# Kernel tuning notes

Measured on AMD Instinct MI355X. Metric: run time of the kernel, lower is better.

The kernel has to match this reference:

```python
import jax, jax.numpy as jnp
import numpy as np

EPS = 1e-5
NUM_HEADS = 12


def setup_inputs() -> dict:
    key = jax.random.key(0)
    ks = jax.random.split(key, 4)
    B, S, E = 8, 1024, 768
    x = jax.random.normal(ks[0], (B, S, E), dtype=jnp.float32)
    ln_w = jnp.ones((E,), dtype=jnp.float32)
    ln_b = jnp.zeros((E,), dtype=jnp.float32)
    # PyTorch packed in-projection [3E, E]; scale ~ Xavier-ish
    in_proj_w = jax.random.normal(ks[1], (3 * E, E), dtype=jnp.float32) * (1.0 / np.sqrt(E))
    in_proj_b = jnp.zeros((3 * E,), dtype=jnp.float32)
    out_proj_w = jax.random.normal(ks[2], (E, E), dtype=jnp.float32) * (1.0 / np.sqrt(E))
    out_proj_b = jnp.zeros((E,), dtype=jnp.float32)
    return {"x": x, "ln_w": ln_w, "ln_b": ln_b,
            "in_proj_w": in_proj_w, "in_proj_b": in_proj_b,
            "out_proj_w": out_proj_w, "out_proj_b": out_proj_b}


def reference(x, ln_w, ln_b, in_proj_w, in_proj_b, out_proj_w, out_proj_b):
    B, S, E = x.shape
    H = NUM_HEADS
    D = E // H
    # LayerNorm over last dim (eps matches torch default 1e-5)
    mu = jnp.mean(x, axis=-1, keepdims=True)
    var = jnp.mean((x - mu) ** 2, axis=-1, keepdims=True)
    xn = (x - mu) * jax.lax.rsqrt(var + EPS) * ln_w + ln_b
    # Packed QKV projection: [B,S,3E]
    qkv = jnp.einsum('bse,fe->bsf', xn, in_proj_w) + in_proj_b
    q, k, v = jnp.split(qkv, 3, axis=-1)
    # [B,H,S,D]
    q = q.reshape(B, S, H, D).transpose(0, 2, 1, 3)
    k = k.reshape(B, S, H, D).transpose(0, 2, 1, 3)
    v = v.reshape(B, S, H, D).transpose(0, 2, 1, 3)
    scale = 1.0 / jnp.sqrt(jnp.asarray(D, dtype=x.dtype))
    # Explicit scores [B,H,S,S] — matches the non-flash need_weights path
    scores = jnp.einsum('bhqd,bhkd->bhqk', q * scale, k)
    attn = jax.nn.softmax(scores, axis=-1)
    ctx = jnp.einsum('bhqk,bhkd->bhqd', attn, v)  # [B,H,S,D]
    ctx = ctx.transpose(0, 2, 1, 3).reshape(B, S, E)
    out = jnp.einsum('bse,fe->bsf', ctx, out_proj_w) + out_proj_b
    return out
```

## Files before the change

### kernel.cpp

```cpp
#include <hip/hip_runtime.h>
#include <cstdint>

typedef _Float16 half8 __attribute__((ext_vector_type(8)));
typedef _Float16 half4v __attribute__((ext_vector_type(4)));
typedef float f32x4 __attribute__((ext_vector_type(4)));

#define AS1(p) (const __attribute__((address_space(1))) void*)(p)
#define AS3(p) (__attribute__((address_space(3))) void*)(p)

__device__ __forceinline__ void gl_lds16(const _Float16* g, _Float16* l) {
  __builtin_amdgcn_global_load_lds(AS1(g), AS3(l), 16, 0, 0);
}

__device__ __forceinline__ f32x4 mfma16(half8 a, half8 b, f32x4 c) {
  return __builtin_amdgcn_mfma_f32_16x16x32_f16(a, b, c, 0, 0, 0);
}

__global__ void conv_f32_f16(const float* __restrict__ s, _Float16* __restrict__ d, int n4) {
  int i = blockIdx.x * 256 + threadIdx.x;
  int stride = gridDim.x * 256;
  for (; i < n4; i += stride) {
    float4 v = ((const float4*)s)[i];
    half4v o = { (_Float16)v.x, (_Float16)v.y, (_Float16)v.z, (_Float16)v.w };
    *(half4v*)(d + (size_t)i * 4) = o;
  }
}

__global__ __launch_bounds__(256) void ln_kernel(const float* __restrict__ x,
    const float* __restrict__ g, const float* __restrict__ be, _Float16* __restrict__ xn) {
  const int row = blockIdx.x, tid = threadIdx.x;
  const float* xr = x + (size_t)row * 768;
  float v0 = xr[tid], v1 = xr[tid + 256], v2 = xr[tid + 512];
  float s = v0 + v1 + v2;
  float ss = v0 * v0 + v1 * v1 + v2 * v2;
  __shared__ float red[8];
  const int w = tid >> 6, l = tid & 63;
  #pragma unroll
  for (int o = 32; o > 0; o >>= 1) { s += __shfl_down(s, o); ss += __shfl_down(ss, o); }
  if (l == 0) { red[w] = s; red[4 + w] = ss; }
  __syncthreads();
  s  = red[0] + red[1] + red[2] + red[3];
  ss = red[4] + red[5] + red[6] + red[7];
  float mu = s * (1.0f / 768.0f);
  float var = ss * (1.0f / 768.0f) - mu * mu;
  float rs = rsqrtf(var + 1e-5f);
  _Float16* xo = xn + (size_t)row * 768;
  xo[tid]       = (_Float16)((v0 - mu) * rs * g[tid]       + be[tid]);
  xo[tid + 256] = (_Float16)((v1 - mu) * rs * g[tid + 256] + be[tid + 256]);
  xo[tid + 512] = (_Float16)((v2 - mu) * rs * g[tid + 512] + be[tid + 512]);
}

template<int EPI>
__global__ __launch_bounds__(256) void gemm_bt(
    const _Float16* __restrict__ A, const _Float16* __restrict__ Bw,
    const float* __restrict__ bias,
    _Float16* __restrict__ qh, _Float16* __restrict__ kh, _Float16* __restrict__ vh,
    float* __restrict__ outp, int M, int N, int K) {
  __shared__ _Float16 As[128 * 32];
  __shared__ _Float16 Bs[128 * 32];
  const int tid = threadIdx.x;
  const int w = tid >> 6, l = tid & 63;
  const int wr = w >> 1, wc = w & 1;
  const int l15 = l & 15, lg = l >> 4;
  const int bn = blockIdx.x, bm = blockIdx.y;
  const _Float16* Ab = A + (size_t)bm * 128 * K;
  const _Float16* Bb = Bw + (size_t)bn * 128 * K;
  f32x4 acc[4][4];
  #pragma unroll
  for (int m = 0; m < 4; ++m)
    #pragma unroll
    for (int n = 0; n < 4; ++n) acc[m][n] = (f32x4){0.f, 0.f, 0.f, 0.f};

  for (int kt = 0; kt < K; kt += 32) {
    #pragma unroll
    for (int j = 0; j < 2; ++j) {
      const int c = j * 256 + tid;
      const int r = c >> 2, kc = (c & 3) * 8;
      gl_lds16(Ab + (size_t)r * K + kt + kc, &As[(j * 256 + w * 64) * 8]);
      gl_lds16(Bb + (size_t)r * K + kt + kc, &Bs[(j * 256 + w * 64) * 8]);
    }
    __syncthreads();
    half8 af[4], bf[4];
    #pragma unroll
    for (int m = 0; m < 4; ++m) af[m] = *(const half8*)&As[(wr * 64 + m * 16 + l15) * 32 + lg * 8];
    #pragma unroll
    for (int n = 0; n < 4; ++n) bf[n] = *(const half8*)&Bs[(wc * 64 + n * 16 + l15) * 32 + lg * 8];
    #pragma unroll
    for (int m = 0; m < 4; ++m)
      #pragma unroll
      for (int n = 0; n < 4; ++n) acc[m][n] = mfma16(af[m], bf[n], acc[m][n]);
    __syncthreads();
  }

  const int rowb = bm * 128 + wr * 64;
  const int colb = bn * 128 + wc * 64;
  if (EPI == 0) {
    const int t = (bn * 128) / 768;
    _Float16* dst = (t == 0) ? qh : (t == 1) ? kh : vh;
    const float qscale = (t == 0) ? 0.125f : 1.0f;
    #pragma unroll
    for (int m = 0; m < 4; ++m)
      #pragma unroll
      for (int n = 0; n < 4; ++n)
        #pragma unroll
        for (int r = 0; r < 4; ++r) {
          const int gr = rowb + m * 16 + lg * 4 + r;
          const int f  = colb + n * 16 + l15;
          const float val = (acc[m][n][r] + bias[f]) * qscale;
          const int fb = f - t * 768;
          const int hh = fb >> 6, dd = fb & 63;
          const int b_ = gr >> 10, s_ = gr & 1023;
          dst[(((size_t)b_ * 12 + hh) * 1024 + s_) * 64 + dd] = (_Float16)val;
        }
  } else {
    #pragma unroll
    for (int m = 0; m < 4; ++m)
      #pragma unroll
      for (int n = 0; n < 4; ++n)
        #pragma unroll
        for (int r = 0; r < 4; ++r) {
          const int gr = rowb + m * 16 + lg * 4 + r;
          const int f  = colb + n * 16 + l15;
          outp[(size_t)gr * 768 + f] = acc[m][n][r] + bias[f];
        }
  }
}

__global__ __launch_bounds__(256) void transpose_v(const _Float16* __restrict__ v,
                                                   _Float16* __restrict__ vt) {
  __shared__ _Float16 t[64][72];
  const int scb = blockIdx.x, bh = blockIdx.y;
  const int tid = threadIdx.x;
  const _Float16* vp = v + (size_t)bh * 1024 * 64 + (size_t)scb * 64 * 64;
  #pragma unroll
  for (int j = 0; j < 2; ++j) {
    const int c = j * 256 + tid;
    const int r = c >> 3, d = (c & 7) * 8;
    *(half8*)&t[r][d] = *(const half8*)&vp[(size_t)r * 64 + d];
  }
  __syncthreads();
  #pragma unroll
  for (int j = 0; j < 2; ++j) {
    const int c = j * 256 + tid;
    const int d = c >> 3, s0 = (c & 7) * 8;
    half8 o;
    #pragma unroll
    for (int x = 0; x < 8; ++x) o[x] = t[s0 + x][d];
    *(half8*)&vt[((size_t)bh * 64 + d) * 1024 + scb * 64 + s0] = o;
  }
}

__global__ __launch_bounds__(256) void attn_fused(
    const _Float16* __restrict__ qg, const _Float16* __restrict__ kg,
    const _Float16* __restrict__ vtg, _Float16* __restrict__ ctx) {
  __shared__ _Float16 Kt[64 * 72];
  __shared__ _Float16 Vt[64 * 72];
  __shared__ _Float16 Pt[128 * 72];
  const int qt = blockIdx.x, bh = blockIdx.y;
  const int b_ = bh / 12, h = bh % 12;
  const _Float16* qp = qg + (size_t)bh * 1024 * 64 + (size_t)qt * 128 * 64;
  const _Float16* kp = kg + (size_t)bh * 1024 * 64;
  const _Float16* vp = vtg + (size_t)bh * 64 * 1024;
  const int tid = threadIdx.x, w = tid >> 6, l = tid & 63;
  const int l15 = l & 15, lg = l >> 4;

  #pragma unroll
  for (int j = 0; j < 4; ++j) {
    const int c = j * 256 + tid;
    const int r = c >> 3, dc = (c & 7) * 8;
    *(half8*)&Pt[r * 72 + dc] = *(const half8*)&qp[(size_t)r * 64 + dc];
  }
  __syncthreads();
  half8 qa[2][2];
  #pragma unroll
  for (int m = 0; m < 2; ++m)
    #pragma unroll
    for (int kk = 0; kk < 2; ++kk)
      qa[m][kk] = *(const half8*)&Pt[(w * 32 + m * 16 + l15) * 72 + kk * 32 + lg * 8];
  __syncthreads();

  f32x4 acc[2][4];
  float Mx[2][4], Lx[2][4];
  #pragma unroll
  for (int m = 0; m < 2; ++m)
    #pragma unroll
    for (int n = 0; n < 4; ++n) acc[m][n] = (f32x4){0.f, 0.f, 0.f, 0.f};
  #pragma unroll
  for (int m = 0; m < 2; ++m)
    #pragma unroll
    for (int r = 0; r < 4; ++r) { Mx[m][r] = -1e30f; Lx[m][r] = 0.f; }

  for (int kt = 0; kt < 16; ++kt) {
    #pragma unroll
    for (int j = 0; j < 2; ++j) {
      const int c = j * 256 + tid;
      const int r = c >> 3, dc = (c & 7) * 8;
      *(half8*)&Kt[r * 72 + dc] = *(const half8*)&kp[((size_t)kt * 64 + r) * 64 + dc];
      *(half8*)&Vt[r * 72 + dc] = *(const half8*)&vp[(size_t)r * 1024 + kt * 64 + dc];
    }
    __syncthreads();

    f32x4 sc[2][4];
    #pragma unroll
    for (int m = 0; m < 2; ++m)
      #pragma unroll
      for (int n = 0; n < 4; ++n) sc[m][n] = (f32x4){0.f, 0.f, 0.f, 0.f};
    #pragma unroll
    for (int n = 0; n < 4; ++n)
      #pragma unroll
      for (int kk = 0; kk < 2; ++kk) {
        const half8 kb = *(const half8*)&Kt[(n * 16 + l15) * 72 + kk * 32 + lg * 8];
        #pragma unroll
        for (int m = 0; m < 2; ++m) sc[m][n] = mfma16(qa[m][kk], kb, sc[m][n]);
      }

    #pragma unroll
    for (int m = 0; m < 2; ++m)
      #pragma unroll
      for (int r = 0; r < 4; ++r) {
        float mx = fmaxf(fmaxf(sc[m][0][r], sc[m][1][r]), fmaxf(sc[m][2][r], sc[m][3][r]));
        #pragma unroll
        for (int o = 1; o < 16; o <<= 1) mx = fmaxf(mx, __shfl_xor(mx, o));
        const float mn = fmaxf(Mx[m][r], mx);
        const float fr = __expf(Mx[m][r] - mn);
        float sum = 0.f;
        #pragma unroll
        for (int n = 0; n < 4; ++n) {
          const float p = __expf(sc[m][n][r] - mn);
          sc[m][n][r] = p;
          sum += p;
        }
        #pragma unroll
        for (int o = 1; o < 16; o <<= 1) sum += __shfl_xor(sum, o);
        Lx[m][r] = Lx[m][r] * fr + sum;
        Mx[m][r] = mn;
        #pragma unroll
        for (int nd = 0; nd < 4; ++nd) acc[m][nd][r] *= fr;
      }

    #pragma unroll
    for (int m = 0; m < 2; ++m)
      #pragma unroll
      for (int n = 0; n < 4; ++n)
        #pragma unroll
        for (int r = 0; r < 4; ++r)
          Pt[(w * 32 + m * 16 + lg * 4 + r) * 72 + n * 16 + l15] = (_Float16)sc[m][n][r];
    __syncthreads();

    #pragma unroll
    for (int kk = 0; kk < 2; ++kk) {
      half8 pa[2];
      #pragma unroll
      for (int m = 0; m < 2; ++m)
        pa[m] = *(const half8*)&Pt[(w * 32 + m * 16 + l15) * 72 + kk * 32 + lg * 8];
      #pragma unroll
      for (int nd = 0; nd < 4; ++nd) {
        const half8 vb = *(const half8*)&Vt[(nd * 16 + l15) * 72 + kk * 32 + lg * 8];
        #pragma unroll
        for (int m = 0; m < 2; ++m) acc[m][nd] = mfma16(pa[m], vb, acc[m][nd]);
      }
    }
    __syncthreads();
  }

  #pragma unroll
  for (int m = 0; m < 2; ++m)
    #pragma unroll
    for (int nd = 0; nd < 4; ++nd)
      #pragma unroll
      for (int r = 0; r < 4; ++r) {
        const int rl = w * 32 + m * 16 + lg * 4 + r;
        const int s_ = qt * 128 + rl;
        const int dd = nd * 16 + l15;
        const float o = acc[m][nd][r] / Lx[m][r];
        ctx[((size_t)b_ * 1024 + s_) * 768 + h * 64 + dd] = (_Float16)o;
      }
}

extern "C" void kernel_launch(void* const* d_in, const int* in_sizes, int n_in,
                              void* d_out, int out_size, void* d_ws, size_t ws_size,
                              hipStream_t stream) {
  const float* x     = (const float*)d_in[0];
  const float* ln_w  = (const float*)d_in[1];
  const float* ln_b  = (const float*)d_in[2];
  const float* w_in  = (const float*)d_in[3];
  const float* b_in  = (const float*)d_in[4];
  const float* w_out = (const float*)d_in[5];
  const float* b_out = (const float*)d_in[6];
  float* out = (float*)d_out;

  _Float16* ws = (_Float16*)d_ws;
  const size_t SZ = (size_t)8192 * 768;
  _Float16* xn   = ws;
  _Float16* wi16 = xn + SZ;
  _Float16* wo16 = wi16 + (size_t)2304 * 768;
  _Float16* qh   = wo16 + (size_t)768 * 768;
  _Float16* kh   = qh + SZ;
  _Float16* vh   = kh + SZ;
  _Float16* vth  = vh + SZ;
  _Float16* ctxh = vth + SZ;

  conv_f32_f16<<<1024, 256, 0, stream>>>(w_in, wi16, (2304 * 768) / 4);
  conv_f32_f16<<<576, 256, 0, stream>>>(w_out, wo16, (768 * 768) / 4);
  ln_kernel<<<8192, 256, 0, stream>>>(x, ln_w, ln_b, xn);
  gemm_bt<0><<<dim3(18, 64), 256, 0, stream>>>(xn, wi16, b_in, qh, kh, vh, nullptr, 8192, 2304, 768);
  transpose_v<<<dim3(16, 96), 256, 0, stream>>>(vh, vth);
  attn_fused<<<dim3(8, 96), 256, 0, stream>>>(qh, kh, vth, ctxh);
  gemm_bt<1><<<dim3(6, 64), 256, 0, stream>>>(ctxh, wo16, b_out, nullptr, nullptr, nullptr, out, 8192, 768, 768);
}
```

Measured before the change: 278.6 us.

## Prefetch K/V tiles into registers and transpose QK MFMA for per-lane softmax

Result: faster. 255.1 us (-8.4%).

```diff
diff --git a/kernel.cpp b/kernel.cpp
--- a/kernel.cpp
+++ b/kernel.cpp
@@ -97,7 +97,7 @@
   if (EPI == 0) {
     const int t = (bn * 128) / 768;
     _Float16* dst = (t == 0) ? qh : (t == 1) ? kh : vh;
-    const float qscale = (t == 0) ? 0.125f : 1.0f;
+    const float qscale = (t == 0) ? 0.125f * 1.44269504088896f : 1.0f;
     #pragma unroll
     for (int m = 0; m < 4; ++m)
       #pragma unroll
@@ -163,6 +163,8 @@
   const _Float16* vp = vtg + (size_t)bh * 64 * 1024;
   const int tid = threadIdx.x, w = tid >> 6, l = tid & 63;
   const int l15 = l & 15, lg = l >> 4;
+  const int cs = (tid >> 3);
+  const int cd = (tid & 7) * 8;
 
   #pragma unroll
   for (int j = 0; j < 4; ++j) {
@@ -177,26 +179,36 @@
     #pragma unroll
     for (int kk = 0; kk < 2; ++kk)
       qa[m][kk] = *(const half8*)&Pt[(w * 32 + m * 16 + l15) * 72 + kk * 32 + lg * 8];
-  __syncthreads();
 
   f32x4 acc[2][4];
-  float Mx[2][4], Lx[2][4];
-  #pragma unroll
-  for (int m = 0; m < 2; ++m)
+  float Mx[2], Lx[2];
+  #pragma unroll
+  for (int m = 0; m < 2; ++m) {
     #pragma unroll
     for (int n = 0; n < 4; ++n) acc[m][n] = (f32x4){0.f, 0.f, 0.f, 0.f};
-  #pragma unroll
-  for (int m = 0; m < 2; ++m)
-    #pragma unroll
-    for (int r = 0; r < 4; ++r) { Mx[m][r] = -1e30f; Lx[m][r] = 0.f; }
+    Mx[m] = -1e30f; Lx[m] = 0.f;
+  }
+
+  half8 kr[2], vr[2];
+  #pragma unroll
+  for (int j = 0; j < 2; ++j) {
+    kr[j] = *(const half8*)&kp[(size_t)(cs + j * 32) * 64 + cd];
+    vr[j] = *(const half8*)&vp[(size_t)(cs + j * 32) * 1024 + cd];
+  }
 
   for (int kt = 0; kt < 16; ++kt) {
+    __syncthreads();
     #pragma unroll
     for (int j = 0; j < 2; ++j) {
-      const int c = j * 256 + tid;
-      const int r = c >> 3, dc = (c & 7) * 8;
-      *(half8*)&Kt[r * 72 + dc] = *(const half8*)&kp[((size_t)kt * 64 + r) * 64 + dc];
-      *(half8*)&Vt[r * 72 + dc] = *(const half8*)&vp[(size_t)r * 1024 + kt * 64 + dc];
+      *(half8*)&Kt[(cs + j * 32) * 72 + cd] = kr[j];
+      *(half8*)&Vt[(cs + j * 32) * 72 + cd] = vr[j];
+    }
+    if (kt < 15) {
+      #pragma unroll
+      for (int j = 0; j < 2; ++j) {
+        kr[j] = *(const half8*)&kp[((size_t)(kt + 1) * 64 + cs + j * 32) * 64 + cd];
+        vr[j] = *(const half8*)&vp[(size_t)(cs + j * 32) * 1024 + (kt + 1) * 64 + cd];
+      }
     }
     __syncthreads();
 
@@ -211,41 +223,48 @@
       for (int kk = 0; kk < 2; ++kk) {
         const half8 kb = *(const half8*)&Kt[(n * 16 + l15) * 72 + kk * 32 + lg * 8];
         #pragma unroll
-        for (int m = 0; m < 2; ++m) sc[m][n] = mfma16(qa[m][kk], kb, sc[m][n]);
-      }
+        for (int m = 0; m < 2; ++m) sc[m][n] = mfma16(kb, qa[m][kk], sc[m][n]);
+      }
+
+    float frm[2];
+    #pragma unroll
+    for (int m = 0; m < 2; ++m) {
+      float mx = sc[m][0][0];
+      #pragma unroll
+      for (int n = 0; n < 4; ++n)
+        #pragma unroll
+        for (int r = 0; r < 4; ++r) mx = fmaxf(mx, sc[m][n][r]);
+      mx = fmaxf(mx, __shfl_xor(mx, 16));
+      mx = fmaxf(mx, __shfl_xor(mx, 32));
+      const float mn = fmaxf(Mx[m], mx);
+      const float fr = exp2f(Mx[m] - mn);
+      Mx[m] = mn;
+      float sum = 0.f;
+      #pragma unroll
+      for (int n = 0; n < 4; ++n) {
+        half4v ph;
+        #pragma unroll
+        for (int r = 0; r < 4; ++r) {
+          const float p = exp2f(sc[m][n][r] - mn);
+          sum += p;
+          ph[r] = (_Float16)p;
+        }
+        *(half4v*)&Pt[(w * 32 + m * 16 + l15) * 72 + n * 16 + lg * 4] = ph;
+      }
+      sum += __shfl_xor(sum, 16);
+      sum += __shfl_xor(sum, 32);
+      Lx[m] = Lx[m] * fr + sum;
+      frm[m] = fr;
+    }
 
     #pragma unroll
     for (int m = 0; m < 2; ++m)
       #pragma unroll
       for (int r = 0; r < 4; ++r) {
-        float mx = fmaxf(fmaxf(sc[m][0][r], sc[m][1][r]), fmaxf(sc[m][2][r], sc[m][3][r]));
-        #pragma unroll
-        for (int o = 1; o < 16; o <<= 1) mx = fmaxf(mx, __shfl_xor(mx, o));
-        const float mn = fmaxf(Mx[m][r], mx);
-        const float fr = __expf(Mx[m][r] - mn);
-        float sum = 0.f;
-        #pragma unroll
-        for (int n = 0; n < 4; ++n) {
-          const float p = __expf(sc[m][n][r] - mn);
-          sc[m][n][r] = p;
-          sum += p;
-        }
-        #pragma unroll
-        for (int o = 1; o < 16; o <<= 1) sum += __shfl_xor(sum, o);
-        Lx[m][r] = Lx[m][r] * fr + sum;
-        Mx[m][r] = mn;
-        #pragma unroll
-        for (int nd = 0; nd < 4; ++nd) acc[m][nd][r] *= fr;
-      }
-
-    #pragma unroll
-    for (int m = 0; m < 2; ++m)
-      #pragma unroll
-      for (int n = 0; n < 4; ++n)
-        #pragma unroll
-        for (int r = 0; r < 4; ++r)
-          Pt[(w * 32 + m * 16 + lg * 4 + r) * 72 + n * 16 + l15] = (_Float16)sc[m][n][r];
-    __syncthreads();
+        const float f = __shfl(frm[m], lg * 4 + r);
+        #pragma unroll
+        for (int nd = 0; nd < 4; ++nd) acc[m][nd][r] *= f;
+      }
 
     #pragma unroll
     for (int kk = 0; kk < 2; ++kk) {
@@ -260,9 +279,13 @@
         for (int m = 0; m < 2; ++m) acc[m][nd] = mfma16(pa[m], vb, acc[m][nd]);
       }
     }
-    __syncthreads();
-  }
-
+  }
+
+  float rv[2][4];
+  #pragma unroll
+  for (int m = 0; m < 2; ++m)
+    #pragma unroll
+    for (int r = 0; r < 4; ++r) rv[m][r] = 1.0f / __shfl(Lx[m], lg * 4 + r);
   #pragma unroll
   for (int m = 0; m < 2; ++m)
     #pragma unroll
@@ -272,7 +295,7 @@
         const int rl = w * 32 + m * 16 + lg * 4 + r;
         const int s_ = qt * 128 + rl;
         const int dd = nd * 16 + l15;
-        const float o = acc[m][nd][r] / Lx[m][r];
+        const float o = acc[m][nd][r] * rv[m][r];
         ctx[((size_t)b_ * 1024 + s_) * 768 + h * 64 + dd] = (_Float16)o;
       }
 }
```
